# Optimization experiments

Measured on AMD Instinct MI355X. Metric: run time of the kernel, lower is better.

The kernel has to match this reference:

```python
import jax, jax.numpy as jnp
from jax import lax
import numpy as np

THRESH = 0.5   # LIF firing threshold (STBP defaults)
LENS = 0.5     # surrogate-gradient window half-width
DECAY = 0.2    # membrane decay
EPS = 1e-5

N_NODES = 20000
C_IN = 128
C_OUT = 64
T = 8
E = 160000


@jax.custom_vjp
def spike_fn(u):
    return (u > THRESH).astype(u.dtype)

def _spike_fwd(u):
    return spike_fn(u), u

def _spike_bwd(u, g):
    # rectangular surrogate: grad passes where |u - thresh| < lens
    return (g * (jnp.abs(u - THRESH) < LENS).astype(g.dtype),)

spike_fn.defvjp(_spike_fwd, _spike_bwd)


def setup_inputs() -> dict:
    key = jax.random.key(0)
    k1, k2, k3, k4, k5 = jax.random.split(key, 5)
    x = jax.random.normal(k1, (N_NODES, C_IN, T), dtype=jnp.float32)
    edge_index = jax.random.randint(k2, (2, E), 0, N_NODES, dtype=jnp.int64)
    gamma = jnp.ones((C_IN,), dtype=jnp.float32)
    beta = jnp.zeros((C_IN,), dtype=jnp.float32)
    s0 = 1.0 / np.sqrt(C_IN)
    W0 = jax.random.uniform(k3, (C_OUT, C_IN), jnp.float32, -s0, s0)  # k=0 hop weights
    W1 = jax.random.uniform(k4, (C_OUT, C_IN), jnp.float32, -s0, s0)  # k=1 hop weights
    b = jax.random.uniform(k5, (C_OUT,), jnp.float32, -s0, s0)
    return {"x": x, "edge_index": edge_index, "gamma": gamma, "beta": beta,
            "W0": W0, "W1": W1, "b": b}


def _ebnorm(x, gamma, beta):
    # BatchNorm1d over [N, C, T]: stats per channel across nodes and time
    mean = jnp.mean(x, axis=(0, 2), keepdims=True)
    var = jnp.mean((x - mean) ** 2, axis=(0, 2), keepdims=True)
    return gamma[None, :, None] * (x - mean) * lax.rsqrt(var + EPS) + beta[None, :, None]


def _lif(x):
    # x: [N, C, T]; iterate membrane over time with reset-by-subtraction-free STBP dynamics
    xt = jnp.moveaxis(x, -1, 0)  # [T, N, C]
    zeros = jnp.zeros_like(xt[0])

    def step(carry, inp):
        mem, sp = carry
        mem = mem * DECAY * (1.0 - sp) + inp
        sp = spike_fn(mem)
        return (mem, sp), sp

    _, spikes = lax.scan(step, (zeros, zeros), xt)
    return jnp.moveaxis(spikes, 0, -1)  # [N, C, T]


def _tagconv(x, edge_index, W0, W1, b):
    # TAGConv K=1 with GCN normalization (no self loops), applied per time step
    src, dst = edge_index[0], edge_index[1]
    n = x.shape[0]
    deg = jax.ops.segment_sum(jnp.ones_like(dst, dtype=x.dtype), dst, num_segments=n)
    dinv = jnp.where(deg > 0, lax.rsqrt(jnp.maximum(deg, 1e-12)), 0.0)
    w = dinv[src] * dinv[dst]                       # [E]
    msg = x[src] * w[:, None, None]                 # [E, C, T]
    agg = jax.ops.segment_sum(msg, dst, num_segments=n)  # [N, C, T]
    out = jnp.einsum('nct,dc->ndt', x, W0) + jnp.einsum('nct,dc->ndt', agg, W1)
    return out + b[None, :, None]


def reference(x, edge_index, gamma, beta, W0, W1, b):
    h = _ebnorm(x, gamma, beta)
    s = _lif(h)
    return _tagconv(s, edge_index, W0, W1, b)
```

## Files before the change

### kernel.cpp

```cpp
#include <hip/hip_runtime.h>
#include <stdint.h>
#include <math.h>

#define N_NODES 20000
#define C_IN 128
#define C_OUT 64
#define T_STEPS 8
#define NE 160000
#define NB_STATS 1024
#define NB_DEG ((NE + 255) / 256)
#define NPB 8
#define RPAD 264

typedef __attribute__((ext_vector_type(8))) short short8;
typedef __attribute__((ext_vector_type(4))) float f32x4;

static __device__ __forceinline__ unsigned short bf16_rne(float f) {
  unsigned u = __builtin_bit_cast(unsigned, f);
  return (unsigned short)((u + 0x7FFFu + ((u >> 16) & 1u)) >> 16);
}

__global__ __launch_bounds__(256) void stats_deg_kernel(const float* __restrict__ x,
                                                        double* __restrict__ dsum,
                                                        double* __restrict__ dsq,
                                                        const int* __restrict__ ei,
                                                        int* __restrict__ deg) {
  int tid = threadIdx.x;
  if (blockIdx.x >= NB_STATS) {
    int e = (blockIdx.x - NB_STATS) * 256 + tid;
    if (e < NE) atomicAdd(&deg[ei[NE + e]], 1);
    return;
  }
  const int P = N_NODES * C_IN;
  int gid = blockIdx.x * 256 + tid;
  double s = 0.0, q = 0.0;
  for (int p = gid; p < P; p += 256 * NB_STATS) {
    const float4* xp = (const float4*)(x + (size_t)p * 8);
    float4 a = xp[0], b = xp[1];
    float v[8] = {a.x, a.y, a.z, a.w, b.x, b.y, b.z, b.w};
#pragma unroll
    for (int j = 0; j < 8; ++j) { double d = (double)v[j]; s += d; q += d * d; }
  }
  __shared__ double ls[256], lq[256];
  ls[tid] = s; lq[tid] = q;
  __syncthreads();
  if (tid < 128) {
    dsum[tid * NB_STATS + blockIdx.x] = ls[tid] + ls[tid + 128];
    dsq [tid * NB_STATS + blockIdx.x] = lq[tid] + lq[tid + 128];
  }
}

__global__ __launch_bounds__(256) void finalize_wtb_kernel(const double* __restrict__ dsum,
                                                           const double* __restrict__ dsq,
                                                           const float* __restrict__ gamma,
                                                           const float* __restrict__ beta,
                                                           double* __restrict__ adbl,
                                                           double* __restrict__ bdbl,
                                                           const float* __restrict__ W0,
                                                           const float* __restrict__ W1,
                                                           unsigned short* __restrict__ WTb) {
  int tid = threadIdx.x;
  if (blockIdx.x >= 128) {
    int idx = (blockIdx.x - 128) * 256 + tid;
    int mt = idx >> 9, kt = (idx >> 6) & 7, lane = idx & 63;
    int m = mt * 16 + (lane & 15);
    int kb = kt * 32 + (lane >> 4) * 8;
    unsigned short frag[8];
#pragma unroll
    for (int j = 0; j < 8; ++j) {
      int k = kb + j;
      float wv = (k < 128) ? W0[m * 128 + k] : W1[m * 128 + (k - 128)];
      frag[j] = bf16_rne(wv);
    }
    *(uint4*)&WTb[(size_t)idx * 8] = *(uint4*)frag;
    return;
  }
  int c = blockIdx.x;
  __shared__ double ls[256], lq[256];
  double s = 0.0, q = 0.0;
#pragma unroll
  for (int i = 0; i < NB_STATS / 256; ++i) {
    s += dsum[c * NB_STATS + tid + 256 * i];
    q += dsq [c * NB_STATS + tid + 256 * i];
  }
  ls[tid] = s; lq[tid] = q;
  __syncthreads();
  for (int o = 128; o > 0; o >>= 1) {
    if (tid < o) { ls[tid] += ls[tid + o]; lq[tid] += lq[tid + o]; }
    __syncthreads();
  }
  if (tid == 0) {
    const double cnt = (double)N_NODES * T_STEPS;
    double mean = ls[0] / cnt;
    double var  = lq[0] / cnt - mean * mean;
    double ai = (double)gamma[c] / sqrt(var + 1e-5);
    adbl[c] = ai;
    bdbl[c] = (double)beta[c] - mean * ai;
  }
}

__global__ __launch_bounds__(256) void lif_kernel(const float* __restrict__ x,
                                                  const double* __restrict__ adbl,
                                                  const double* __restrict__ bdbl,
                                                  unsigned char* __restrict__ spk) {
  int p = blockIdx.x * 256 + threadIdx.x;
  int c = p & (C_IN - 1);
  const float4* xp = (const float4*)(x + (size_t)p * 8);
  float4 a4 = xp[0], b4 = xp[1];
  float v[8] = {a4.x, a4.y, a4.z, a4.w, b4.x, b4.y, b4.z, b4.w};
  double a = adbl[c], bb = bdbl[c];
  double mem = 0.0, sp = 0.0;
  unsigned byte = 0;
#pragma unroll
  for (int t = 0; t < 8; ++t) {
    double h = a * (double)v[t] + bb;
    mem = mem * (0.2 * (1.0 - sp)) + h;
    int fire = mem > 0.5;
    sp = fire ? 1.0 : 0.0;
    byte |= (unsigned)fire << t;
  }
  spk[p] = (unsigned char)byte;
}

__global__ __launch_bounds__(1024) void scan_kernel(const int* __restrict__ deg,
                                                    int* __restrict__ offs,
                                                    int* __restrict__ cursor,
                                                    float* __restrict__ dinv) {
  int tid = threadIdx.x, lane = tid & 63, w = tid >> 6;
  int base = tid * 20;
  int v[20];
  int s = 0;
#pragma unroll
  for (int i = 0; i < 20; ++i) {
    int n = base + i;
    int d = (n < N_NODES) ? deg[n] : 0;
    v[i] = d; s += d;
  }
  int p = s;
#pragma unroll
  for (int o = 1; o < 64; o <<= 1) {
    int u = __shfl_up(p, o);
    if (lane >= o) p += u;
  }
  __shared__ int wsum[16];
  if (lane == 63) wsum[w] = p;
  __syncthreads();
  int wpre = 0;
  for (int j = 0; j < w; ++j) wpre += wsum[j];
  int excl = wpre + p - s;
#pragma unroll
  for (int i = 0; i < 20; ++i) {
    int n = base + i;
    if (n < N_NODES) {
      offs[n] = excl; cursor[n] = excl;
      dinv[n] = v[i] > 0 ? (float)(1.0 / sqrt((double)v[i])) : 0.f;
      excl += v[i];
    }
  }
  if (tid == 1023) offs[N_NODES] = excl;
}

__global__ __launch_bounds__(256) void fill_kernel(const int* __restrict__ ei,
                                                   int* __restrict__ cursor,
                                                   int* __restrict__ csr) {
  int e = blockIdx.x * 256 + threadIdx.x;
  if (e < NE) {
    int pos = atomicAdd(&cursor[ei[NE + e]], 1);
    csr[pos] = ei[e];
  }
}

__global__ __launch_bounds__(512) void main_kernel(const unsigned char* __restrict__ spk,
                                                   const int* __restrict__ offs,
                                                   const int* __restrict__ csr,
                                                   const float* __restrict__ dinv,
                                                   const unsigned short* __restrict__ WTb,
                                                   const float* __restrict__ bias,
                                                   float* __restrict__ out) {
  __shared__ unsigned short Bls[64 * RPAD];
  int tid = threadIdx.x;
  int n0 = blockIdx.x * NPB;
  int lane = tid & 63, w = tid >> 6;

  {
    int col = tid & 63, cg = tid >> 6;
    int node = n0 + (col >> 3), t = col & 7;
    uint4 u = *(const uint4*)(spk + (size_t)node * 128 + cg * 16);
    unsigned ua[4] = {u.x, u.y, u.z, u.w};
    unsigned ow[8];
#pragma unroll
    for (int i = 0; i < 4; ++i) {
      unsigned vv = (ua[i] >> t) & 0x01010101u;
      unsigned s0 = (vv & 1u)         ? 0x3F80u : 0u;
      unsigned s1 = ((vv >> 8) & 1u)  ? 0x3F800000u : 0u;
      unsigned s2 = ((vv >> 16) & 1u) ? 0x3F80u : 0u;
      unsigned s3 = (vv >> 24)        ? 0x3F800000u : 0u;
      ow[i * 2]     = s0 | s1;
      ow[i * 2 + 1] = s2 | s3;
    }
    uint4 o0 = {ow[0], ow[1], ow[2], ow[3]};
    uint4 o1 = {ow[4], ow[5], ow[6], ow[7]};
    *(uint4*)&Bls[col * RPAD + cg * 16]     = o0;
    *(uint4*)&Bls[col * RPAD + cg * 16 + 8] = o1;
  }

  {
    int node = n0 + w;
    int e0 = offs[node], e1 = offs[node + 1];
    const unsigned short* sp16 = (const unsigned short*)spk;
    float acc[16];
#pragma unroll
    for (int j = 0; j < 16; ++j) acc[j] = 0.f;
    int e = e0;
#pragma unroll 1
    for (; e + 4 <= e1; e += 4) {
      int s0 = csr[e], s1 = csr[e + 1], s2 = csr[e + 2], s3 = csr[e + 3];
      float w0 = dinv[s0], w1 = dinv[s1], w2 = dinv[s2], w3 = dinv[s3];
      unsigned b0 = sp16[(size_t)s0 * 64 + lane];
      unsigned b1 = sp16[(size_t)s1 * 64 + lane];
      unsigned b2 = sp16[(size_t)s2 * 64 + lane];
      unsigned b3 = sp16[(size_t)s3 * 64 + lane];
#pragma unroll
      for (int j = 0; j < 16; ++j) {
        acc[j] = fmaf((float)((b0 >> j) & 1u), w0, acc[j]);
        acc[j] = fmaf((float)((b1 >> j) & 1u), w1, acc[j]);
        acc[j] = fmaf((float)((b2 >> j) & 1u), w2, acc[j]);
        acc[j] = fmaf((float)((b3 >> j) & 1u), w3, acc[j]);
      }
    }
#pragma unroll 1
    for (; e < e1; ++e) {
      int src = csr[e];
      float wt = dinv[src];
      unsigned bits = sp16[(size_t)src * 64 + lane];
#pragma unroll
      for (int j = 0; j < 16; ++j)
        acc[j] = fmaf((float)((bits >> j) & 1u), wt, acc[j]);
    }
    float sc = dinv[node];
    int colb = w * 8;
    int c0 = 2 * lane;
#pragma unroll
    for (int t = 0; t < 8; ++t) {
      unsigned pk = (unsigned)bf16_rne(acc[t] * sc) |
                    ((unsigned)bf16_rne(acc[8 + t] * sc) << 16);
      *(unsigned*)&Bls[(colb + t) * RPAD + 128 + c0] = pk;
    }
  }
  __syncthreads();

  int q = lane >> 4, l16 = lane & 15;
  int mt = w & 3, ct0 = w >> 2, ct1 = ct0 + 2;
  int colA = ct0 * 16 + l16, colB = ct1 * 16 + l16;
  const short8* WT8 = (const short8*)WTb;
  f32x4 acc0 = {0, 0, 0, 0}, acc1 = {0, 0, 0, 0};
#pragma unroll
  for (int kt = 0; kt < 8; ++kt) {
    short8 a = WT8[(mt * 8 + kt) * 64 + lane];
    short8 bA = *(const short8*)&Bls[colA * RPAD + kt * 32 + q * 8];
    short8 bB = *(const short8*)&Bls[colB * RPAD + kt * 32 + q * 8];
    acc0 = __builtin_amdgcn_mfma_f32_16x16x32_bf16(a, bA, acc0, 0, 0, 0);
    acc1 = __builtin_amdgcn_mfma_f32_16x16x32_bf16(a, bB, acc1, 0, 0, 0);
  }

  int nodeA = n0 + (colA >> 3), tA = colA & 7;
  int nodeB = n0 + (colB >> 3), tB = colB & 7;
  float* obA = out + (size_t)nodeA * 512 + tA;
  float* obB = out + (size_t)nodeB * 512 + tB;
#pragma unroll
  for (int r = 0; r < 4; ++r) {
    int d = mt * 16 + q * 4 + r;
    float bv = bias[d];
    obA[d * 8] = acc0[r] + bv;
    obB[d * 8] = acc1[r] + bv;
  }
}

extern "C" void kernel_launch(void* const* d_in, const int* in_sizes, int n_in,
                              void* d_out, int out_size, void* d_ws, size_t ws_size,
                              hipStream_t stream) {
  const float* x     = (const float*)d_in[0];
  const int*   ei    = (const int*)d_in[1];
  const float* gamma = (const float*)d_in[2];
  const float* beta  = (const float*)d_in[3];
  const float* W0    = (const float*)d_in[4];
  const float* W1    = (const float*)d_in[5];
  const float* bias  = (const float*)d_in[6];
  float* out = (float*)d_out;

  char* ws = (char*)d_ws;
  size_t off = 0;
  auto alloc = [&](size_t bytes) -> void* {
    void* p = ws + off;
    off = (off + bytes + 255) & ~(size_t)255;
    return p;
  };
  double* dsum = (double*)alloc(128 * NB_STATS * 8);
  double* dsq  = (double*)alloc(128 * NB_STATS * 8);
  double* adbl = (double*)alloc(128 * 8);
  double* bdbl = (double*)alloc(128 * 8);
  int*    deg  = (int*)alloc(N_NODES * 4);
  float*  dinv = (float*)alloc(N_NODES * 4);
  int*    offs = (int*)alloc((N_NODES + 1) * 4);
  int*    curs = (int*)alloc(N_NODES * 4);
  int*    csr  = (int*)alloc(NE * 4);
  unsigned char* spk = (unsigned char*)alloc((size_t)N_NODES * C_IN);
  unsigned short* WTb = (unsigned short*)alloc(2048 * 8 * 2);

  hipMemsetAsync(deg, 0, N_NODES * 4, stream);

  stats_deg_kernel<<<NB_STATS + NB_DEG, 256, 0, stream>>>(x, dsum, dsq, ei, deg);
  finalize_wtb_kernel<<<128 + 8, 256, 0, stream>>>(dsum, dsq, gamma, beta, adbl, bdbl, W0, W1, WTb);
  lif_kernel<<<(N_NODES * C_IN) / 256, 256, 0, stream>>>(x, adbl, bdbl, spk);
  scan_kernel<<<1, 1024, 0, stream>>>(deg, offs, curs, dinv);
  fill_kernel<<<(NE + 255) / 256, 256, 0, stream>>>(ei, curs, csr);
  main_kernel<<<N_NODES / NPB, 512, 0, stream>>>(spk, offs, csr, dinv, WTb, bias, out);
}
```

Baseline: 235.8 us.

## Merge preprocessing kernels to cut launches from six to four

The weight-fragment conversion moves into the stats/degree kernel, the degree prefix scan into the BN finalize kernel, and the CSR fill into the LIF kernel. This removes two kernel launches and their serialization gaps by running independent work in the same grid. The scan now runs as a single 256-thread block with serial 79-element loops that read deg twice, which may lengthen the critical path of the finalize kernel. Degree blocks are also moved ahead of the stats blocks so the atomics start early.

```diff
diff --git a/kernel.cpp b/kernel.cpp
--- a/kernel.cpp
+++ b/kernel.cpp
@@ -9,6 +9,7 @@
 #define NE 160000
 #define NB_STATS 1024
 #define NB_DEG ((NE + 255) / 256)
+#define NB_LIF ((N_NODES * C_IN) / 256)
 #define NPB 8
 #define RPAD 264
 
@@ -20,19 +21,38 @@
   return (unsigned short)((u + 0x7FFFu + ((u >> 16) & 1u)) >> 16);
 }
 
-__global__ __launch_bounds__(256) void stats_deg_kernel(const float* __restrict__ x,
-                                                        double* __restrict__ dsum,
-                                                        double* __restrict__ dsq,
-                                                        const int* __restrict__ ei,
-                                                        int* __restrict__ deg) {
+__global__ __launch_bounds__(256) void stats_deg_wtb_kernel(const float* __restrict__ x,
+                                                            double* __restrict__ dsum,
+                                                            double* __restrict__ dsq,
+                                                            const int* __restrict__ ei,
+                                                            int* __restrict__ deg,
+                                                            const float* __restrict__ W0,
+                                                            const float* __restrict__ W1,
+                                                            unsigned short* __restrict__ WTb) {
   int tid = threadIdx.x;
-  if (blockIdx.x >= NB_STATS) {
-    int e = (blockIdx.x - NB_STATS) * 256 + tid;
+  if (blockIdx.x < NB_DEG) {
+    int e = blockIdx.x * 256 + tid;
     if (e < NE) atomicAdd(&deg[ei[NE + e]], 1);
     return;
   }
+  if (blockIdx.x >= NB_DEG + NB_STATS) {
+    int idx = (blockIdx.x - NB_DEG - NB_STATS) * 256 + tid;
+    int mt = idx >> 9, kt = (idx >> 6) & 7, lane = idx & 63;
+    int m = mt * 16 + (lane & 15);
+    int kb = kt * 32 + (lane >> 4) * 8;
+    unsigned short frag[8];
+#pragma unroll
+    for (int j = 0; j < 8; ++j) {
+      int k = kb + j;
+      float wv = (k < 128) ? W0[m * 128 + k] : W1[m * 128 + (k - 128)];
+      frag[j] = bf16_rne(wv);
+    }
+    *(uint4*)&WTb[(size_t)idx * 8] = *(uint4*)frag;
+    return;
+  }
+  int sb = blockIdx.x - NB_DEG;
   const int P = N_NODES * C_IN;
-  int gid = blockIdx.x * 256 + tid;
+  int gid = sb * 256 + tid;
   double s = 0.0, q = 0.0;
   for (int p = gid; p < P; p += 256 * NB_STATS) {
     const float4* xp = (const float4*)(x + (size_t)p * 8);
@@ -45,34 +65,54 @@
   ls[tid] = s; lq[tid] = q;
   __syncthreads();
   if (tid < 128) {
-    dsum[tid * NB_STATS + blockIdx.x] = ls[tid] + ls[tid + 128];
-    dsq [tid * NB_STATS + blockIdx.x] = lq[tid] + lq[tid + 128];
-  }
-}
-
-__global__ __launch_bounds__(256) void finalize_wtb_kernel(const double* __restrict__ dsum,
-                                                           const double* __restrict__ dsq,
-                                                           const float* __restrict__ gamma,
-                                                           const float* __restrict__ beta,
-                                                           double* __restrict__ adbl,
-                                                           double* __restrict__ bdbl,
-                                                           const float* __restrict__ W0,
-                                                           const float* __restrict__ W1,
-                                                           unsigned short* __restrict__ WTb) {
+    dsum[tid * NB_STATS + sb] = ls[tid] + ls[tid + 128];
+    dsq [tid * NB_STATS + sb] = lq[tid] + lq[tid + 128];
+  }
+}
+
+__global__ __launch_bounds__(256) void finalize_scan_kernel(const double* __restrict__ dsum,
+                                                            const double* __restrict__ dsq,
+                                                            const float* __restrict__ gamma,
+                                                            const float* __restrict__ beta,
+                                                            double* __restrict__ adbl,
+                                                            double* __restrict__ bdbl,
+                                                            const int* __restrict__ deg,
+                                                            int* __restrict__ offs,
+                                                            int* __restrict__ cursor,
+                                                            float* __restrict__ dinv) {
   int tid = threadIdx.x;
-  if (blockIdx.x >= 128) {
-    int idx = (blockIdx.x - 128) * 256 + tid;
-    int mt = idx >> 9, kt = (idx >> 6) & 7, lane = idx & 63;
-    int m = mt * 16 + (lane & 15);
-    int kb = kt * 32 + (lane >> 4) * 8;
-    unsigned short frag[8];
-#pragma unroll
-    for (int j = 0; j < 8; ++j) {
-      int k = kb + j;
-      float wv = (k < 128) ? W0[m * 128 + k] : W1[m * 128 + (k - 128)];
-      frag[j] = bf16_rne(wv);
-    }
-    *(uint4*)&WTb[(size_t)idx * 8] = *(uint4*)frag;
+  if (blockIdx.x == 128) {
+    int lane = tid & 63, w = tid >> 6;
+    int base = tid * 79;
+    int s = 0;
+#pragma unroll 1
+    for (int i = 0; i < 79; ++i) {
+      int n = base + i;
+      if (n < N_NODES) s += deg[n];
+    }
+    int p = s;
+#pragma unroll
+    for (int o = 1; o < 64; o <<= 1) {
+      int u = __shfl_up(p, o);
+      if (lane >= o) p += u;
+    }
+    __shared__ int wsum[4];
+    if (lane == 63) wsum[w] = p;
+    __syncthreads();
+    int wpre = 0;
+    for (int j = 0; j < w; ++j) wpre += wsum[j];
+    int run = wpre + p - s;
+#pragma unroll 1
+    for (int i = 0; i < 79; ++i) {
+      int n = base + i;
+      if (n < N_NODES) {
+        int d = deg[n];
+        offs[n] = run; cursor[n] = run;
+        dinv[n] = d > 0 ? (float)(1.0 / sqrt((double)d)) : 0.f;
+        run += d;
+      }
+    }
+    if (tid == 0) offs[N_NODES] = wsum[0] + wsum[1] + wsum[2] + wsum[3];
     return;
   }
   int c = blockIdx.x;
@@ -99,11 +139,23 @@
   }
 }
 
-__global__ __launch_bounds__(256) void lif_kernel(const float* __restrict__ x,
-                                                  const double* __restrict__ adbl,
-                                                  const double* __restrict__ bdbl,
-                                                  unsigned char* __restrict__ spk) {
-  int p = blockIdx.x * 256 + threadIdx.x;
+__global__ __launch_bounds__(256) void lif_fill_kernel(const float* __restrict__ x,
+                                                       const double* __restrict__ adbl,
+                                                       const double* __restrict__ bdbl,
+                                                       unsigned char* __restrict__ spk,
+                                                       const int* __restrict__ ei,
+                                                       int* __restrict__ cursor,
+                                                       int* __restrict__ csr) {
+  int tid = threadIdx.x;
+  if (blockIdx.x >= NB_LIF) {
+    int e = (blockIdx.x - NB_LIF) * 256 + tid;
+    if (e < NE) {
+      int pos = atomicAdd(&cursor[ei[NE + e]], 1);
+      csr[pos] = ei[e];
+    }
+    return;
+  }
+  int p = blockIdx.x * 256 + tid;
   int c = p & (C_IN - 1);
   const float4* xp = (const float4*)(x + (size_t)p * 8);
   float4 a4 = xp[0], b4 = xp[1];
@@ -120,54 +172,6 @@
     byte |= (unsigned)fire << t;
   }
   spk[p] = (unsigned char)byte;
-}
-
-__global__ __launch_bounds__(1024) void scan_kernel(const int* __restrict__ deg,
-                                                    int* __restrict__ offs,
-                                                    int* __restrict__ cursor,
-                                                    float* __restrict__ dinv) {
-  int tid = threadIdx.x, lane = tid & 63, w = tid >> 6;
-  int base = tid * 20;
-  int v[20];
-  int s = 0;
-#pragma unroll
-  for (int i = 0; i < 20; ++i) {
-    int n = base + i;
-    int d = (n < N_NODES) ? deg[n] : 0;
-    v[i] = d; s += d;
-  }
-  int p = s;
-#pragma unroll
-  for (int o = 1; o < 64; o <<= 1) {
-    int u = __shfl_up(p, o);
-    if (lane >= o) p += u;
-  }
-  __shared__ int wsum[16];
-  if (lane == 63) wsum[w] = p;
-  __syncthreads();
-  int wpre = 0;
-  for (int j = 0; j < w; ++j) wpre += wsum[j];
-  int excl = wpre + p - s;
-#pragma unroll
-  for (int i = 0; i < 20; ++i) {
-    int n = base + i;
-    if (n < N_NODES) {
-      offs[n] = excl; cursor[n] = excl;
-      dinv[n] = v[i] > 0 ? (float)(1.0 / sqrt((double)v[i])) : 0.f;
-      excl += v[i];
-    }
-  }
-  if (tid == 1023) offs[N_NODES] = excl;
-}
-
-__global__ __launch_bounds__(256) void fill_kernel(const int* __restrict__ ei,
-                                                   int* __restrict__ cursor,
-                                                   int* __restrict__ csr) {
-  int e = blockIdx.x * 256 + threadIdx.x;
-  if (e < NE) {
-    int pos = atomicAdd(&cursor[ei[NE + e]], 1);
-    csr[pos] = ei[e];
-  }
 }
 
 __global__ __launch_bounds__(512) void main_kernel(const unsigned char* __restrict__ spk,
@@ -309,10 +313,9 @@
 
   hipMemsetAsync(deg, 0, N_NODES * 4, stream);
 
-  stats_deg_kernel<<<NB_STATS + NB_DEG, 256, 0, stream>>>(x, dsum, dsq, ei, deg);
-  finalize_wtb_kernel<<<128 + 8, 256, 0, stream>>>(dsum, dsq, gamma, beta, adbl, bdbl, W0, W1, WTb);
-  lif_kernel<<<(N_NODES * C_IN) / 256, 256, 0, stream>>>(x, adbl, bdbl, spk);
-  scan_kernel<<<1, 1024, 0, stream>>>(deg, offs, curs, dinv);
-  fill_kernel<<<(NE + 255) / 256, 256, 0, stream>>>(ei, curs, csr);
+  stats_deg_wtb_kernel<<<NB_DEG + NB_STATS + 8, 256, 0, stream>>>(x, dsum, dsq, ei, deg, W0, W1, WTb);
+  finalize_scan_kernel<<<129, 256, 0, stream>>>(dsum, dsq, gamma, beta, adbl, bdbl,
+                                                deg, offs, curs, dinv);
+  lif_fill_kernel<<<NB_LIF + NB_DEG, 256, 0, stream>>>(x, adbl, bdbl, spk, ei, curs, csr);
   main_kernel<<<N_NODES / NPB, 512, 0, stream>>>(spk, offs, csr, dinv, WTb, bias, out);
 }
```

After: 265.6 us. 12.6% more time.
